# Optimization experiments

Measured on AMD Instinct MI355X. Metric: run time of the kernel, lower is better.

The kernel has to match this reference:

```python
import jax, jax.numpy as jnp
import numpy as np

N = 50000      # rows of A == cols of A (square constraint/variable graph)
NNZ = 1_600_000
D = 128        # x_size == y_size == out_size (forced by the module's wiring)


def spmm(rows, cols, vals, X, n_out):
    # out[r] = sum_{e: rows[e]==r} vals[e] * X[cols[e]]
    return jax.ops.segment_sum(vals[:, None] * X[cols], rows, num_segments=n_out)


def _linear(z, w, b):
    return z @ w.T + b


def setup_inputs() -> dict:
    key = jax.random.key(0)
    ks = jax.random.split(key, 20)
    f = lambda i, shape, s=1.0: jax.random.normal(ks[i], shape, dtype=jnp.float32) * s
    w_scale = 1.0 / np.sqrt(D)
    return {
        "x": f(0, (N, D)),
        "y": f(1, (N, D)),
        "c": f(2, (N, 1)),
        "b": f(3, (N, 1)),
        "A_vals": f(4, (NNZ,)),
        "A_rows": jax.random.randint(ks[5], (NNZ,), 0, N),
        "A_cols": jax.random.randint(ks[6], (NNZ,), 0, N),
        "Ukx_w": f(7, (D, D), w_scale), "Ukx_b": f(8, (D,), w_scale),
        "Uky_w": f(9, (D, D), w_scale), "Uky_b": f(10, (D,), w_scale),
        "tau": f(11, (1,)),
        "Vky_w": f(12, (D, D), w_scale), "Vky_b": f(13, (D,), w_scale),
        "Wkx_w": f(14, (D, D), w_scale), "Wkx_b": f(15, (D,), w_scale),
        "Vkx_w": f(16, (D, D), w_scale), "Vkx_b": f(17, (D,), w_scale),
        "sigma": f(18, (1,)),
    }


def reference(x, y, c, b, A_vals, A_rows, A_cols,
              Ukx_w, Ukx_b, Uky_w, Uky_b, tau,
              Vky_w, Vky_b, Wkx_w, Wkx_b, Vkx_w, Vkx_b, sigma):
    # --- pdhg_layer_x: x <- relu(Ukx(x) - tau * (c @ ones(1,D) - AT @ Uky(y))) ---
    # c @ ones(1, D) is just broadcasting c:[N,1] to [N,D].
    uy = _linear(y, Uky_w, Uky_b)                      # [N, D]
    at_uy = spmm(A_cols, A_rows, A_vals, uy, N)        # AT spmm: swap row/col indices
    x_new = jax.nn.relu(_linear(x, Ukx_w, Ukx_b) - tau * (c - at_uy))

    # --- pdhg_layer_y: y <- relu(Vky(y) - sigma * (b@ones - 2*A@Wkx(x') + A@Vkx(x'))) ---
    wx = _linear(x_new, Wkx_w, Wkx_b)                  # [N, D]
    vx = _linear(x_new, Vkx_w, Vkx_b)                  # [N, D]
    a_wx = spmm(A_rows, A_cols, A_vals, wx, N)
    a_vx = spmm(A_rows, A_cols, A_vals, vx, N)
    y_new = jax.nn.relu(_linear(y, Vky_w, Vky_b) - sigma * (b - 2.0 * a_wx + a_vx))
    return (x_new, y_new)
```

## Files before the change

kernel.cpp:

```cpp
#include <hip/hip_runtime.h>

#define D 128
#define RB 64
#define NBKMAX 1024
#define CH 256

typedef __attribute__((ext_vector_type(4))) float f32x4;
typedef __attribute__((ext_vector_type(8))) short bf16x8;

__device__ __forceinline__ unsigned short bf16r(float f) {
    unsigned b = __float_as_uint(f);
    return (unsigned short)((b + 0x7FFFu + ((b >> 16) & 1u)) >> 16);
}

__global__ __launch_bounds__(256) void setup_weights(
    const float* __restrict__ Uky, const float* __restrict__ Ukx,
    const float* __restrict__ Vky, const float* __restrict__ Vkx,
    const float* __restrict__ Wkx, const float* __restrict__ Vkx_b,
    const float* __restrict__ Wkx_b,
    float* __restrict__ UkyT, float* __restrict__ UkxT,
    float* __restrict__ VkyT, float* __restrict__ WcT,
    unsigned short* __restrict__ UkyB, unsigned short* __restrict__ UkxB,
    unsigned short* __restrict__ VkyB, unsigned short* __restrict__ WcB,
    float* __restrict__ bc)
{
    const int m = blockIdx.x;
    if (m < 4) {
        const float* src = (m == 0) ? Uky : (m == 1) ? Ukx : (m == 2) ? Vky : nullptr;
        float* dst = (m == 0) ? UkyT : (m == 1) ? UkxT : (m == 2) ? VkyT : WcT;
        for (int i = threadIdx.x; i < D * D; i += 256) {
            int k = i >> 7, d = i & 127;
            float v;
            if (m == 3) v = Vkx[d * D + k] - 2.0f * Wkx[d * D + k];
            else        v = src[d * D + k];
            dst[i] = v;
        }
        if (m == 3 && threadIdx.x < D)
            bc[threadIdx.x] = Vkx_b[threadIdx.x] - 2.0f * Wkx_b[threadIdx.x];
    } else {
        const int mm = m - 4;
        const float* src = (mm == 0) ? Uky : (mm == 1) ? Ukx : (mm == 2) ? Vky : nullptr;
        unsigned short* dst = (mm == 0) ? UkyB : (mm == 1) ? UkxB : (mm == 2) ? VkyB : WcB;
        for (int i = threadIdx.x; i < D * D; i += 256) {
            float v;
            if (mm == 3) v = Vkx[i] - 2.0f * Wkx[i];
            else         v = src[i];
            dst[i] = bf16r(v);
        }
    }
}

template <int EPI, int OB16>
__global__ __launch_bounds__(256) void gemm_mfma(
    const float* __restrict__ X, const unsigned short* __restrict__ Wb,
    const float* __restrict__ bias, const float* __restrict__ colvec,
    const float* __restrict__ spout, const float* __restrict__ scal,
    float* __restrict__ out, int N)
{
    __shared__ __align__(16) unsigned short Xs[64 * 128];
    const int t = threadIdx.x;
    const int block_row = blockIdx.x * 64;

#pragma unroll
    for (int i = 0; i < 8; ++i) {
        int f = t + i * 256;
        int r = f >> 5;
        int k4 = (f & 31) << 2;
        float4 g = make_float4(0.f, 0.f, 0.f, 0.f);
        int row = block_row + r;
        if (row < N) g = *reinterpret_cast<const float4*>(&X[(size_t)row * D + k4]);
        ushort4 h;
        h.x = bf16r(g.x); h.y = bf16r(g.y); h.z = bf16r(g.z); h.w = bf16r(g.w);
        unsigned byte = (unsigned)(k4 * 2) ^ ((unsigned)(r & 7) << 4);
        *reinterpret_cast<ushort4*>((char*)Xs + r * 256 + byte) = h;
    }
    __syncthreads();

    const int w  = t >> 6;
    const int l  = t & 63;
    const int lr = l & 15;
    const int lq = l >> 4;

    f32x4 acc[8];
#pragma unroll
    for (int nt = 0; nt < 8; ++nt) acc[nt] = (f32x4)(0.f);

    const int arow = w * 16 + lr;

#pragma unroll
    for (int kc = 0; kc < 4; ++kc) {
        unsigned abyte = ((unsigned)(kc * 64 + lq * 16)) ^ ((unsigned)(arow & 7) << 4);
        bf16x8 a = *reinterpret_cast<const bf16x8*>((const char*)Xs + arow * 256 + abyte);
#pragma unroll
        for (int nt = 0; nt < 8; ++nt) {
            bf16x8 b = *reinterpret_cast<const bf16x8*>(
                &Wb[(size_t)(nt * 16 + lr) * D + kc * 32 + lq * 8]);
            acc[nt] = __builtin_amdgcn_mfma_f32_16x16x32_bf16(a, b, acc[nt], 0, 0, 0);
        }
    }

    const float sc = (EPI == 0) ? 0.f : scal[0];
    float bs[8];
#pragma unroll
    for (int nt = 0; nt < 8; ++nt) bs[nt] = bias[nt * 16 + lr];

#pragma unroll
    for (int r = 0; r < 4; ++r) {
        const int row = block_row + w * 16 + lq * 4 + r;
        if (row >= N) continue;
        const float cv = (EPI == 0) ? 0.f : colvec[row];
#pragma unroll
        for (int nt = 0; nt < 8; ++nt) {
            const int col = nt * 16 + lr;
            float res = acc[nt][r] + bs[nt];
            if (EPI == 1) {
                float sp = spout[(size_t)row * D + col];
                res = fmaxf(res - sc * (cv - sp), 0.f);
            } else if (EPI == 2) {
                float sp = spout[(size_t)row * D + col];
                res = fmaxf(res - sc * (cv + sp), 0.f);
            }
            if (OB16) ((unsigned short*)out)[(size_t)row * D + col] = bf16r(res);
            else      out[(size_t)row * D + col] = res;
        }
    }
}

template <int EPI>
__global__ __launch_bounds__(256) void gemm_v2(
    const float* __restrict__ X, const float* __restrict__ WT,
    const float* __restrict__ bias, const float* __restrict__ colvec,
    const float* __restrict__ spout, const float* __restrict__ scal,
    float* __restrict__ out, int N)
{
    __shared__ float Xsf[64][D + 4];
    __shared__ float Wt[64][D + 4];
    const int t = threadIdx.x;
    const int block_row = blockIdx.x * 64;

#pragma unroll
    for (int i = 0; i < 8; ++i) {
        int f = t + i * 256;
        int r = f >> 5;
        int k4 = (f & 31) << 2;
        float4 g = make_float4(0.f, 0.f, 0.f, 0.f);
        int row = block_row + r;
        if (row < N) g = *reinterpret_cast<const float4*>(&X[(size_t)row * D + k4]);
        *reinterpret_cast<float4*>(&Xsf[r][k4]) = g;
    }

    const int cg = t & 15;
    const int rp = t >> 4;
    const int r0 = rp * 4;
    const int c0 = cg * 4, c1 = 64 + cg * 4;
    float acc[4][8] = {{0.f}};

    for (int kb = 0; kb < D; kb += 64) {
        __syncthreads();
#pragma unroll
        for (int i = 0; i < 8; ++i) {
            int f = t + i * 256;
            int kk = f >> 5;
            int d4 = (f & 31) << 2;
            float4 g = *reinterpret_cast<const float4*>(&WT[(size_t)(kb + kk) * D + d4]);
            *reinterpret_cast<float4*>(&Wt[kk][d4]) = g;
        }
        __syncthreads();
#pragma unroll 2
        for (int k4 = 0; k4 < 64; k4 += 4) {
            float4 xr[4];
#pragma unroll
            for (int j = 0; j < 4; ++j)
                xr[j] = *reinterpret_cast<const float4*>(&Xsf[r0 + j][kb + k4]);
#pragma unroll
            for (int q = 0; q < 4; ++q) {
                const float4 w0 = *reinterpret_cast<const float4*>(&Wt[k4 + q][c0]);
                const float4 w1 = *reinterpret_cast<const float4*>(&Wt[k4 + q][c1]);
#pragma unroll
                for (int j = 0; j < 4; ++j) {
                    const float xv = (q == 0) ? xr[j].x : (q == 1) ? xr[j].y
                                   : (q == 2) ? xr[j].z : xr[j].w;
                    acc[j][0] += xv * w0.x; acc[j][1] += xv * w0.y;
                    acc[j][2] += xv * w0.z; acc[j][3] += xv * w0.w;
                    acc[j][4] += xv * w1.x; acc[j][5] += xv * w1.y;
                    acc[j][6] += xv * w1.z; acc[j][7] += xv * w1.w;
                }
            }
        }
    }

    const float sc = (EPI == 0) ? 0.f : scal[0];
    const float4 bias0 = *reinterpret_cast<const float4*>(&bias[c0]);
    const float4 bias1 = *reinterpret_cast<const float4*>(&bias[c1]);

#pragma unroll
    for (int j = 0; j < 4; ++j) {
        const int row = block_row + r0 + j;
        if (row >= N) continue;
        const float cv = (EPI == 0) ? 0.f : colvec[row];
#pragma unroll
        for (int h = 0; h < 2; ++h) {
            const int col = (h == 0) ? c0 : c1;
            const float4 bsv = (h == 0) ? bias0 : bias1;
            float4 res;
            res.x = acc[j][h * 4 + 0] + bsv.x;
            res.y = acc[j][h * 4 + 1] + bsv.y;
            res.z = acc[j][h * 4 + 2] + bsv.z;
            res.w = acc[j][h * 4 + 3] + bsv.w;
            if (EPI == 1) {
                float4 sp = *reinterpret_cast<const float4*>(&spout[(size_t)row * D + col]);
                res.x = fmaxf(res.x - sc * (cv - sp.x), 0.f);
                res.y = fmaxf(res.y - sc * (cv - sp.y), 0.f);
                res.z = fmaxf(res.z - sc * (cv - sp.z), 0.f);
                res.w = fmaxf(res.w - sc * (cv - sp.w), 0.f);
            } else if (EPI == 2) {
                float4 sp = *reinterpret_cast<const float4*>(&spout[(size_t)row * D + col]);
                res.x = fmaxf(res.x - sc * (cv + sp.x), 0.f);
                res.y = fmaxf(res.y - sc * (cv + sp.y), 0.f);
                res.z = fmaxf(res.z - sc * (cv + sp.z), 0.f);
                res.w = fmaxf(res.w - sc * (cv + sp.w), 0.f);
            }
            *reinterpret_cast<float4*>(&out[(size_t)row * D + col]) = res;
        }
    }
}

__global__ __launch_bounds__(256) void hist_chunks(
    const int* __restrict__ rows, const int* __restrict__ cols,
    int* __restrict__ hR, int* __restrict__ hC, int nnz, int nbk, int ce)
{
    __shared__ int lh[NBKMAX];
    const int chunk = blockIdx.x;
    const bool isC = blockIdx.y;
    const int* idx = isC ? cols : rows;
    int* hout = (isC ? hC : hR) + (size_t)chunk * nbk;
    for (int i = threadIdx.x; i < nbk; i += 256) lh[i] = 0;
    __syncthreads();
    const int e0 = chunk * ce, e1 = min(nnz, e0 + ce);
    for (int e = e0 + threadIdx.x; e < e1; e += 256)
        atomicAdd(&lh[idx[e] >> 6], 1);
    __syncthreads();
    for (int i = threadIdx.x; i < nbk; i += 256) hout[i] = lh[i];
}

__global__ __launch_bounds__(256) void bucket_tot(
    const int* __restrict__ hR, const int* __restrict__ hC,
    int* __restrict__ cntR, int* __restrict__ cntC, int nbk)
{
    const int b = blockIdx.x;
    const bool isC = blockIdx.y;
    const int* h = (isC ? hC : hR);
    __shared__ int s[256];
    int v = h[(size_t)threadIdx.x * nbk + b];
    s[threadIdx.x] = v;
    __syncthreads();
#pragma unroll
    for (int d = 128; d > 0; d >>= 1) {
        if (threadIdx.x < d) s[threadIdx.x] += s[threadIdx.x + d];
        __syncthreads();
    }
    if (threadIdx.x == 0) (isC ? cntC : cntR)[b] = s[0];
}

__global__ __launch_bounds__(256) void scan_buckets(
    const int* __restrict__ cntR, const int* __restrict__ cntC,
    int* __restrict__ goffR, int* __restrict__ goffC, int nbk)
{
    const int* cnt = blockIdx.x ? cntC : cntR;
    int* goff = blockIdx.x ? goffC : goffR;
    __shared__ int s[256];
    const int t = threadIdx.x;
    const int base = t * 4;
    int loc[4]; int sum = 0;
#pragma unroll
    for (int u = 0; u < 4; ++u) {
        int idx = base + u;
        int v = (idx < nbk) ? cnt[idx] : 0;
        loc[u] = sum; sum += v;
    }
    s[t] = sum;
    __syncthreads();
#pragma unroll
    for (int d = 1; d < 256; d <<= 1) {
        int tv = (t >= d) ? s[t - d] : 0;
        __syncthreads();
        s[t] += tv;
        __syncthreads();
    }
    int excl = s[t] - sum;
#pragma unroll
    for (int u = 0; u < 4; ++u) {
        int idx = base + u;
        if (idx < nbk) goff[idx] = excl + loc[u];
    }
}

__global__ __launch_bounds__(256) void runstarts(
    int* __restrict__ hR, int* __restrict__ hC,
    const int* __restrict__ goffR, const int* __restrict__ goffC, int nbk)
{
    const int b = blockIdx.x;
    const bool isC = blockIdx.y;
    int* h = (isC ? hC : hR);
    const int g0 = (isC ? goffC : goffR)[b];
    __shared__ int s[256];
    const int t = threadIdx.x;
    int v = h[(size_t)t * nbk + b];
    s[t] = v;
    __syncthreads();
#pragma unroll
    for (int d = 1; d < 256; d <<= 1) {
        int tv = (t >= d) ? s[t - d] : 0;
        __syncthreads();
        s[t] += tv;
        __syncthreads();
    }
    h[(size_t)t * nbk + b] = g0 + s[t] - v;
}

__global__ __launch_bounds__(1024) void scatter_chunks(
    const int* __restrict__ rows, const int* __restrict__ cols,
    const float* __restrict__ vals,
    const int* __restrict__ rsR, int2* __restrict__ recR,
    const int* __restrict__ rsC, int2* __restrict__ recC,
    int nnz, int nbk, int ce)
{
    __shared__ int lrsR[NBKMAX], lcurR[NBKMAX];
    __shared__ int lrsC[NBKMAX], lcurC[NBKMAX];
    const int chunk = blockIdx.x;
    for (int i = threadIdx.x; i < nbk; i += 1024) {
        lrsR[i] = rsR[(size_t)chunk * nbk + i]; lcurR[i] = 0;
        lrsC[i] = rsC[(size_t)chunk * nbk + i]; lcurC[i] = 0;
    }
    __syncthreads();
    const int e0 = chunk * ce, e1 = min(nnz, e0 + ce);
    for (int e = e0 + threadIdx.x; e < e1; e += 1024) {
        int r = rows[e], c = cols[e];
        int vb = __float_as_int(vals[e]);
        int bR = r >> 6, bC = c >> 6;
        int pR = lrsR[bR] + atomicAdd(&lcurR[bR], 1);
        recR[pR] = make_int2(((r & 63) << 16) | c, vb);
        int pC = lrsC[bC] + atomicAdd(&lcurC[bC], 1);
        recC[pC] = make_int2(((c & 63) << 16) | r, vb);
    }
}

__global__ __launch_bounds__(256) void sort_buckets(
    const int2* __restrict__ recR, const int2* __restrict__ recC,
    const int* __restrict__ goffR, const int* __restrict__ cntR,
    const int* __restrict__ goffC, const int* __restrict__ cntC,
    unsigned* __restrict__ pairsR, unsigned* __restrict__ pairsC,
    int* __restrict__ offR, int* __restrict__ lenR,
    int* __restrict__ offC, int* __restrict__ lenC, int N)
{
    const bool isC = blockIdx.y;
    const int b = blockIdx.x;
    const int2* rec = isC ? recC : recR;
    unsigned* pairs = isC ? pairsC : pairsR;
    int* off = isC ? offC : offR;
    int* len = isC ? lenC : lenR;
    const int s = (isC ? goffC : goffR)[b];
    const int L = (isC ? cntC : cntR)[b];
    const int t = threadIdx.x;

    __shared__ int lcnt[RB], lpos[RB], lcur[RB];
    if (t < RB) lcnt[t] = 0;
    __syncthreads();
    for (int i = t; i < L; i += 256)
        atomicAdd(&lcnt[rec[s + i].x >> 16], 1);
    __syncthreads();
    if (t == 0) {
        int run = 0;
#pragma unroll
        for (int r = 0; r < RB; ++r) { lpos[r] = run; run += lcnt[r]; }
    }
    __syncthreads();
    if (t < RB) {
        int row = b * RB + t;
        if (row < N) { off[row] = s + lpos[t]; len[row] = lcnt[t]; }
        lcur[t] = 0;
    }
    __syncthreads();
    for (int i = t; i < L; i += 256) {
        int2 pr = rec[s + i];
        int r = pr.x >> 16;
        int p = lpos[r] + atomicAdd(&lcur[r], 1);
        unsigned vb = (unsigned)pr.y;
        unsigned v16 = (vb + 0x7FFFu + ((vb >> 16) & 1u)) >> 16;
        pairs[s + p] = (v16 << 16) | (unsigned)(pr.x & 0xFFFF);
    }
}

__global__ __launch_bounds__(256) void spmm_pairs_v3(
    const unsigned* __restrict__ pairs, const int* __restrict__ off,
    const int* __restrict__ len, const unsigned short* __restrict__ Xb,
    float* __restrict__ out, int N)
{
    const int row = (blockIdx.x * 256 + threadIdx.x) >> 6;
    if (row >= N) return;
    const int lane = threadIdx.x & 63;
    const int half = lane >> 5;
    const int cq = (lane & 31) << 2;
    const int s = off[row];
    const int L = len[row];

    float4 a0 = make_float4(0.f, 0.f, 0.f, 0.f);
    float4 a1 = make_float4(0.f, 0.f, 0.f, 0.f);
    float4 a2 = make_float4(0.f, 0.f, 0.f, 0.f);
    float4 a3 = make_float4(0.f, 0.f, 0.f, 0.f);

#define BF(u) __uint_as_float((unsigned)(u) << 16)
    int i = 0;
    for (; i + 7 < L; i += 8) {
        unsigned p0 = pairs[s + i + 0 + half];
        unsigned p1 = pairs[s + i + 2 + half];
        unsigned p2 = pairs[s + i + 4 + half];
        unsigned p3 = pairs[s + i + 6 + half];
        ushort4 x0 = *reinterpret_cast<const ushort4*>(&Xb[(size_t)(p0 & 0xFFFFu) * D + cq]);
        ushort4 x1 = *reinterpret_cast<const ushort4*>(&Xb[(size_t)(p1 & 0xFFFFu) * D + cq]);
        ushort4 x2 = *reinterpret_cast<const ushort4*>(&Xb[(size_t)(p2 & 0xFFFFu) * D + cq]);
        ushort4 x3 = *reinterpret_cast<const ushort4*>(&Xb[(size_t)(p3 & 0xFFFFu) * D + cq]);
        float v0 = __uint_as_float(p0 & 0xFFFF0000u);
        float v1 = __uint_as_float(p1 & 0xFFFF0000u);
        float v2 = __uint_as_float(p2 & 0xFFFF0000u);
        float v3 = __uint_as_float(p3 & 0xFFFF0000u);
        a0.x += v0 * BF(x0.x); a0.y += v0 * BF(x0.y); a0.z += v0 * BF(x0.z); a0.w += v0 * BF(x0.w);
        a1.x += v1 * BF(x1.x); a1.y += v1 * BF(x1.y); a1.z += v1 * BF(x1.z); a1.w += v1 * BF(x1.w);
        a2.x += v2 * BF(x2.x); a2.y += v2 * BF(x2.y); a2.z += v2 * BF(x2.z); a2.w += v2 * BF(x2.w);
        a3.x += v3 * BF(x3.x); a3.y += v3 * BF(x3.y); a3.z += v3 * BF(x3.z); a3.w += v3 * BF(x3.w);
    }
    for (; i < L; i += 2) {
        int e = i + half;
        unsigned p = (e < L) ? pairs[s + e] : 0u;
        ushort4 xv = *reinterpret_cast<const ushort4*>(&Xb[(size_t)(p & 0xFFFFu) * D + cq]);
        float v = __uint_as_float(p & 0xFFFF0000u);
        a0.x += v * BF(xv.x); a0.y += v * BF(xv.y); a0.z += v * BF(xv.z); a0.w += v * BF(xv.w);
    }
#undef BF

    float4 A;
    A.x = (a0.x + a1.x) + (a2.x + a3.x);
    A.y = (a0.y + a1.y) + (a2.y + a3.y);
    A.z = (a0.z + a1.z) + (a2.z + a3.z);
    A.w = (a0.w + a1.w) + (a2.w + a3.w);
    A.x += __shfl_xor(A.x, 32);
    A.y += __shfl_xor(A.y, 32);
    A.z += __shfl_xor(A.z, 32);
    A.w += __shfl_xor(A.w, 32);
    if (half == 0)
        *reinterpret_cast<float4*>(&out[(size_t)row * D + cq]) = A;
}

__global__ __launch_bounds__(256) void spmm_atomic(
    const float* __restrict__ vals, const int* __restrict__ orow,
    const int* __restrict__ gcol, const float* __restrict__ Xm,
    float* __restrict__ outm, int nnz)
{
    const int gwave = (blockIdx.x * 256 + threadIdx.x) >> 6;
    const int lane = threadIdx.x & 63;
    const int e0 = gwave * 4;
#pragma unroll
    for (int i = 0; i < 4; ++i) {
        int e = e0 + i;
        if (e >= nnz) break;
        float v = vals[e];
        int r = orow[e];
        int c = gcol[e];
        float2 xv = *reinterpret_cast<const float2*>(&Xm[(size_t)c * D + lane * 2]);
        unsafeAtomicAdd(&outm[(size_t)r * D + lane * 2 + 0], v * xv.x);
        unsafeAtomicAdd(&outm[(size_t)r * D + lane * 2 + 1], v * xv.y);
    }
}

extern "C" void kernel_launch(void* const* d_in, const int* in_sizes, int n_in,
                              void* d_out, int out_size, void* d_ws, size_t ws_size,
                              hipStream_t stream) {
    const float* x      = (const float*)d_in[0];
    const float* y      = (const float*)d_in[1];
    const float* c      = (const float*)d_in[2];
    const float* b      = (const float*)d_in[3];
    const float* A_vals = (const float*)d_in[4];
    const int*   A_rows = (const int*)d_in[5];
    const int*   A_cols = (const int*)d_in[6];
    const float* Ukx_w  = (const float*)d_in[7];
    const float* Ukx_b  = (const float*)d_in[8];
    const float* Uky_w  = (const float*)d_in[9];
    const float* Uky_b  = (const float*)d_in[10];
    const float* tau    = (const float*)d_in[11];
    const float* Vky_w  = (const float*)d_in[12];
    const float* Vky_b  = (const float*)d_in[13];
    const float* Wkx_w  = (const float*)d_in[14];
    const float* Wkx_b  = (const float*)d_in[15];
    const float* Vkx_w  = (const float*)d_in[16];
    const float* Vkx_b  = (const float*)d_in[17];
    const float* sigma  = (const float*)d_in[18];

    const int N   = in_sizes[0] / D;
    const int nnz = in_sizes[4];
    const int nbk = (N + RB - 1) / RB;

    float* out_x = (float*)d_out;
    float* out_y = out_x + (size_t)N * D;

    const int gemm_grid = (N + 63) / 64;
    const int ggrid = (N + 3) / 4;

    const size_t pool = (size_t)nnz;
    char* base = (char*)d_ws;
    float* tmp = (float*)base;
    int2* recR = (int2*)base;
    int2* recC = recR + pool;
    size_t region0 = (size_t)N * D * 4;
    if (2 * pool * 8 > region0) region0 = 2 * pool * 8;
    char* pers = base + region0;
    float* UkyT = (float*)pers;
    float* UkxT = UkyT + D * D;
    float* VkyT = UkxT + D * D;
    float* WcT  = VkyT + D * D;
    unsigned short* UkyB = (unsigned short*)(WcT + D * D);
    unsigned short* UkxB = UkyB + D * D;
    unsigned short* VkyB = UkxB + D * D;
    unsigned short* WcB  = VkyB + D * D;
    float* bc = (float*)(WcB + D * D);
    unsigned* pairsR = (unsigned*)(bc + D);
    unsigned* pairsC = pairsR + pool;
    int* cntR  = (int*)(pairsC + pool);
    int* cntC  = cntR + nbk;
    int* goffR = cntC + nbk;
    int* goffC = goffR + nbk;
    int* offR  = goffC + nbk;
    int* lenR  = offR + N;
    int* offC  = lenR + N;
    int* lenC  = offC + N;
    int* hR = (int*)pairsR;
    int* hC = hR + (size_t)CH * nbk;

    unsigned short* uyb = (unsigned short*)out_y;
    unsigned short* zxb = (unsigned short*)tmp;

    size_t need = region0 + (4 * (size_t)D * D + D) * 4 + 4 * (size_t)D * D * 2
                + 2 * pool * 4 + (4 * (size_t)nbk + 4 * (size_t)N) * 4;
    bool h_fits = (size_t)2 * CH * nbk * 4 <= pool * 4;

    setup_weights<<<8, 256, 0, stream>>>(Uky_w, Ukx_w, Vky_w, Vkx_w, Wkx_w,
                                         Vkx_b, Wkx_b, UkyT, UkxT, VkyT, WcT,
                                         UkyB, UkxB, VkyB, WcB, bc);

    if (N < 65536 && nbk <= NBKMAX && ws_size >= need && h_fits) {
        const int ce = (nnz + CH - 1) / CH;

        {
            dim3 g1(CH, 2);
            hist_chunks<<<g1, 256, 0, stream>>>(A_rows, A_cols, hR, hC, nnz, nbk, ce);
            dim3 g2(nbk, 2);
            bucket_tot<<<g2, 256, 0, stream>>>(hR, hC, cntR, cntC, nbk);
            scan_buckets<<<2, 256, 0, stream>>>(cntR, cntC, goffR, goffC, nbk);
            runstarts<<<g2, 256, 0, stream>>>(hR, hC, goffR, goffC, nbk);
            scatter_chunks<<<CH, 1024, 0, stream>>>(A_rows, A_cols, A_vals,
                                                    hR, recR, hC, recC, nnz, nbk, ce);
            sort_buckets<<<g2, 256, 0, stream>>>(recR, recC, goffR, cntR, goffC, cntC,
                                                 pairsR, pairsC, offR, lenR, offC, lenC, N);
        }

        gemm_mfma<0, 1><<<gemm_grid, 256, 0, stream>>>(y, UkyB, Uky_b, nullptr, nullptr, nullptr,
                                                       (float*)uyb, N);
        spmm_pairs_v3<<<ggrid, 256, 0, stream>>>(pairsC, offC, lenC, uyb, out_x, N);
        gemm_mfma<1, 0><<<gemm_grid, 256, 0, stream>>>(x, UkxB, Ukx_b, c, out_x, tau, out_x, N);
        gemm_mfma<0, 1><<<gemm_grid, 256, 0, stream>>>(out_x, WcB, bc, nullptr, nullptr, nullptr,
                                                       (float*)zxb, N);
        spmm_pairs_v3<<<ggrid, 256, 0, stream>>>(pairsR, offR, lenR, zxb, out_y, N);
        gemm_mfma<2, 0><<<gemm_grid, 256, 0, stream>>>(y, VkyB, Vky_b, b, out_y, sigma, out_y, N);
    } else {
        const int spmm_grid = (nnz + 15) / 16;
        gemm_v2<0><<<gemm_grid, 256, 0, stream>>>(y, UkyT, Uky_b, nullptr, nullptr, nullptr, tmp, N);
        hipMemsetAsync(out_x, 0, (size_t)N * D * sizeof(float), stream);
        spmm_atomic<<<spmm_grid, 256, 0, stream>>>(A_vals, A_cols, A_rows, tmp, out_x, nnz);
        gemm_v2<1><<<gemm_grid, 256, 0, stream>>>(x, UkxT, Ukx_b, c, out_x, tau, out_x, N);
        gemm_v2<0><<<gemm_grid, 256, 0, stream>>>(out_x, WcT, bc, nullptr, nullptr, nullptr, tmp, N);
        hipMemsetAsync(out_y, 0, (size_t)N * D * sizeof(float), stream);
        spmm_atomic<<<spmm_grid, 256, 0, stream>>>(A_vals, A_rows, A_cols, tmp, out_y, nnz);
        gemm_v2<2><<<gemm_grid, 256, 0, stream>>>(y, VkyT, Vky_b, b, out_y, sigma, out_y, N);
    }
}
```

Measured before the change: 293.9 us.

## Widen row buckets and stage chunk scatter through LDS for coalesced writes

```diff
diff --git a/kernel.cpp b/kernel.cpp
--- a/kernel.cpp
+++ b/kernel.cpp
@@ -1,9 +1,10 @@
 #include <hip/hip_runtime.h>
 
 #define D 128
-#define RB 64
-#define NBKMAX 1024
+#define RB 256
+#define NBKMAX 256
 #define CH 256
+#define LDSREC 6400
 
 typedef __attribute__((ext_vector_type(4))) float f32x4;
 typedef __attribute__((ext_vector_type(8))) short bf16x8;
@@ -238,7 +239,7 @@
     __syncthreads();
     const int e0 = chunk * ce, e1 = min(nnz, e0 + ce);
     for (int e = e0 + threadIdx.x; e < e1; e += 256)
-        atomicAdd(&lh[idx[e] >> 6], 1);
+        atomicAdd(&lh[idx[e] >> 8], 1);
     __syncthreads();
     for (int i = threadIdx.x; i < nbk; i += 256) hout[i] = lh[i];
 }
@@ -270,15 +271,8 @@
     int* goff = blockIdx.x ? goffC : goffR;
     __shared__ int s[256];
     const int t = threadIdx.x;
-    const int base = t * 4;
-    int loc[4]; int sum = 0;
-#pragma unroll
-    for (int u = 0; u < 4; ++u) {
-        int idx = base + u;
-        int v = (idx < nbk) ? cnt[idx] : 0;
-        loc[u] = sum; sum += v;
-    }
-    s[t] = sum;
+    int v = (t < nbk) ? cnt[t] : 0;
+    s[t] = v;
     __syncthreads();
 #pragma unroll
     for (int d = 1; d < 256; d <<= 1) {
@@ -287,21 +281,18 @@
         s[t] += tv;
         __syncthreads();
     }
-    int excl = s[t] - sum;
-#pragma unroll
-    for (int u = 0; u < 4; ++u) {
-        int idx = base + u;
-        if (idx < nbk) goff[idx] = excl + loc[u];
-    }
+    if (t < nbk) goff[t] = s[t] - v;
 }
 
 __global__ __launch_bounds__(256) void runstarts(
-    int* __restrict__ hR, int* __restrict__ hC,
+    const int* __restrict__ hR, const int* __restrict__ hC,
+    int* __restrict__ rsR, int* __restrict__ rsC,
     const int* __restrict__ goffR, const int* __restrict__ goffC, int nbk)
 {
     const int b = blockIdx.x;
     const bool isC = blockIdx.y;
-    int* h = (isC ? hC : hR);
+    const int* h = (isC ? hC : hR);
+    int* rs = (isC ? rsC : rsR);
     const int g0 = (isC ? goffC : goffR)[b];
     __shared__ int s[256];
     const int t = threadIdx.x;
@@ -315,33 +306,63 @@
         s[t] += tv;
         __syncthreads();
     }
-    h[(size_t)t * nbk + b] = g0 + s[t] - v;
-}
-
-__global__ __launch_bounds__(1024) void scatter_chunks(
+    rs[(size_t)t * nbk + b] = g0 + s[t] - v;
+}
+
+__global__ __launch_bounds__(256) void scatter_sorted(
     const int* __restrict__ rows, const int* __restrict__ cols,
     const float* __restrict__ vals,
-    const int* __restrict__ rsR, int2* __restrict__ recR,
-    const int* __restrict__ rsC, int2* __restrict__ recC,
+    const int* __restrict__ hR, const int* __restrict__ rsR, int2* __restrict__ recR,
+    const int* __restrict__ hC, const int* __restrict__ rsC, int2* __restrict__ recC,
     int nnz, int nbk, int ce)
 {
-    __shared__ int lrsR[NBKMAX], lcurR[NBKMAX];
-    __shared__ int lrsC[NBKMAX], lcurC[NBKMAX];
+    __shared__ int2 recL[LDSREC];
+    __shared__ int lpos[NBKMAX], lcur[NBKMAX], lrs[NBKMAX], ssc[256];
+    const int t = threadIdx.x;
     const int chunk = blockIdx.x;
-    for (int i = threadIdx.x; i < nbk; i += 1024) {
-        lrsR[i] = rsR[(size_t)chunk * nbk + i]; lcurR[i] = 0;
-        lrsC[i] = rsC[(size_t)chunk * nbk + i]; lcurC[i] = 0;
-    }
-    __syncthreads();
     const int e0 = chunk * ce, e1 = min(nnz, e0 + ce);
-    for (int e = e0 + threadIdx.x; e < e1; e += 1024) {
-        int r = rows[e], c = cols[e];
-        int vb = __float_as_int(vals[e]);
-        int bR = r >> 6, bC = c >> 6;
-        int pR = lrsR[bR] + atomicAdd(&lcurR[bR], 1);
-        recR[pR] = make_int2(((r & 63) << 16) | c, vb);
-        int pC = lrsC[bC] + atomicAdd(&lcurC[bC], 1);
-        recC[pC] = make_int2(((c & 63) << 16) | r, vb);
+    const int Lc = e1 - e0;
+
+#pragma unroll
+    for (int g = 0; g < 2; ++g) {
+        const int* h  = g ? hC : hR;
+        const int* rs = g ? rsC : rsR;
+        int2* recG    = g ? recC : recR;
+
+        int v = (t < nbk) ? h[(size_t)chunk * nbk + t] : 0;
+        if (t < nbk) lrs[t] = rs[(size_t)chunk * nbk + t];
+        ssc[t] = v;
+        __syncthreads();
+#pragma unroll
+        for (int d = 1; d < 256; d <<= 1) {
+            int tv = (t >= d) ? ssc[t - d] : 0;
+            __syncthreads();
+            ssc[t] += tv;
+            __syncthreads();
+        }
+        if (t < nbk) { lpos[t] = ssc[t] - v; lcur[t] = 0; }
+        __syncthreads();
+
+        for (int e = e0 + t; e < e1; e += 256) {
+            int r = rows[e], c = cols[e];
+            int dst = g ? c : r;
+            int gcol = g ? r : c;
+            int b = dst >> 8;
+            int q = atomicAdd(&lcur[b], 1);
+            recL[lpos[b] + q] = make_int2(((dst & 255) << 16) | gcol,
+                                          __float_as_int(vals[e]));
+        }
+        __syncthreads();
+
+        for (int j = t; j < Lc; j += 256) {
+            int lo = 0, hi = nbk - 1;
+            while (lo < hi) {
+                int mid = (lo + hi + 1) >> 1;
+                if (lpos[mid] <= j) lo = mid; else hi = mid - 1;
+            }
+            recG[lrs[lo] + (j - lpos[lo])] = recL[j];
+        }
+        __syncthreads();
     }
 }
 
@@ -364,18 +385,18 @@
     const int t = threadIdx.x;
 
     __shared__ int lcnt[RB], lpos[RB], lcur[RB];
-    if (t < RB) lcnt[t] = 0;
+    lcnt[t] = 0;
     __syncthreads();
     for (int i = t; i < L; i += 256)
         atomicAdd(&lcnt[rec[s + i].x >> 16], 1);
     __syncthreads();
     if (t == 0) {
         int run = 0;
-#pragma unroll
+#pragma unroll 8
         for (int r = 0; r < RB; ++r) { lpos[r] = run; run += lcnt[r]; }
     }
     __syncthreads();
-    if (t < RB) {
+    {
         int row = b * RB + t;
         if (row < N) { off[row] = s + lpos[t]; len[row] = lcnt[t]; }
         lcur[t] = 0;
@@ -504,6 +525,7 @@
 
     const int gemm_grid = (N + 63) / 64;
     const int ggrid = (N + 3) / 4;
+    const int ce = (nnz + CH - 1) / CH;
 
     const size_t pool = (size_t)nnz;
     char* base = (char*)d_ws;
@@ -532,32 +554,33 @@
     int* lenR  = offR + N;
     int* offC  = lenR + N;
     int* lenC  = offC + N;
-    int* hR = (int*)pairsR;
-    int* hC = hR + (size_t)CH * nbk;
+    int* hR  = (int*)pairsR;
+    int* hC  = hR + (size_t)CH * nbk;
+    int* rsR = hC + (size_t)CH * nbk;
+    int* rsC = rsR + (size_t)CH * nbk;
 
     unsigned short* uyb = (unsigned short*)out_y;
     unsigned short* zxb = (unsigned short*)tmp;
 
     size_t need = region0 + (4 * (size_t)D * D + D) * 4 + 4 * (size_t)D * D * 2
                 + 2 * pool * 4 + (4 * (size_t)nbk + 4 * (size_t)N) * 4;
-    bool h_fits = (size_t)2 * CH * nbk * 4 <= pool * 4;
+    bool alias_fits = (size_t)4 * CH * nbk * 4 <= pool * 4;
 
     setup_weights<<<8, 256, 0, stream>>>(Uky_w, Ukx_w, Vky_w, Vkx_w, Wkx_w,
                                          Vkx_b, Wkx_b, UkyT, UkxT, VkyT, WcT,
                                          UkyB, UkxB, VkyB, WcB, bc);
 
-    if (N < 65536 && nbk <= NBKMAX && ws_size >= need && h_fits) {
-        const int ce = (nnz + CH - 1) / CH;
-
+    if (N < 65536 && nbk <= NBKMAX && ws_size >= need && alias_fits && ce <= LDSREC) {
         {
             dim3 g1(CH, 2);
             hist_chunks<<<g1, 256, 0, stream>>>(A_rows, A_cols, hR, hC, nnz, nbk, ce);
             dim3 g2(nbk, 2);
             bucket_tot<<<g2, 256, 0, stream>>>(hR, hC, cntR, cntC, nbk);
             scan_buckets<<<2, 256, 0, stream>>>(cntR, cntC, goffR, goffC, nbk);
-            runstarts<<<g2, 256, 0, stream>>>(hR, hC, goffR, goffC, nbk);
-            scatter_chunks<<<CH, 1024, 0, stream>>>(A_rows, A_cols, A_vals,
-                                                    hR, recR, hC, recC, nnz, nbk, ce);
+            runstarts<<<g2, 256, 0, stream>>>(hR, hC, rsR, rsC, goffR, goffC, nbk);
+            scatter_sorted<<<CH, 256, 0, stream>>>(A_rows, A_cols, A_vals,
+                                                   hR, rsR, recR, hC, rsC, recC,
+                                                   nnz, nbk, ce);
             sort_buckets<<<g2, 256, 0, stream>>>(recR, recC, goffR, cntR, goffC, cntC,
                                                  pairsR, pairsC, offR, lenR, offC, lenC, N);
         }
```

New measurement: 327.7 us. 1.12x slower.
